# Kernel tuning notes

Measured on AMD Instinct MI355X. Metric: run time of the kernel, lower is better.

Reference implementation:

```python
import jax, jax.numpy as jnp
import numpy as np
import math

N_EMBD = 1024
N_HEAD = 16
HEAD_DIM = N_EMBD // N_HEAD


def setup_inputs() -> dict:
    key = jax.random.key(0)
    k_x, k_w1, k_b1, k_w2, k_b2 = jax.random.split(key, 5)
    B, T = 2, 2048
    x = jax.random.normal(k_x, (B, T, N_EMBD), dtype=jnp.float32)
    # ln1: Linear(n_embd, 3*n_embd); weights stored as [in, out] for x @ W
    W_qkv = jax.random.normal(k_w1, (N_EMBD, 3 * N_EMBD), dtype=jnp.float32) * 0.02
    b_qkv = jax.random.normal(k_b1, (3 * N_EMBD,), dtype=jnp.float32) * 0.02
    # ln2: Linear(n_embd, n_embd)
    W_out = jax.random.normal(k_w2, (N_EMBD, N_EMBD), dtype=jnp.float32) * 0.02
    b_out = jax.random.normal(k_b2, (N_EMBD,), dtype=jnp.float32) * 0.02
    return {"x": x, "W_qkv": W_qkv, "b_qkv": b_qkv, "W_out": W_out, "b_out": b_out}


def reference(x, W_qkv, b_qkv, W_out, b_out):
    B, T, C = x.shape
    qkv = x @ W_qkv + b_qkv                      # [B,T,3C]
    q, k, v = jnp.split(qkv, 3, axis=-1)
    # reshape to heads: [B, H, T, D]
    def to_heads(t):
        return t.reshape(B, T, N_HEAD, HEAD_DIM).transpose(0, 2, 1, 3)
    Q, K, V = to_heads(q), to_heads(k), to_heads(v)
    # NOTE: scale is 1/sqrt(n_head), as in the source (not sqrt(head_dim));
    # NOTE: no causal mask is applied, faithfully matching the source forward.
    scale = 1.0 / math.sqrt(N_HEAD)
    scores = jnp.einsum('bhqd,bhkd->bhqk', Q, K) * scale  # [B,H,T,T]
    attn = jax.nn.softmax(scores, axis=-1)
    out = jnp.einsum('bhqk,bhkd->bhqd', attn, V)          # [B,H,T,D]
    out = out.transpose(0, 2, 1, 3).reshape(B, T, C)
    # dropout = 0.0 -> identity (eval mode)
    return out @ W_out + b_out
```

## Files before the change

kernel.cpp:

```cpp
#include <hip/hip_runtime.h>
#include <hip/hip_bf16.h>
#include <stdint.h>

typedef __bf16 bf16_t;
typedef __bf16 bf16x8 __attribute__((ext_vector_type(8)));
typedef float  f32x4  __attribute__((ext_vector_type(4)));

#define AS1 __attribute__((address_space(1)))
#define AS3 __attribute__((address_space(3)))

__device__ __forceinline__ void gload16(const bf16_t* g, char* l) {
  __builtin_amdgcn_global_load_lds((AS1 const void*)(uintptr_t)g, (AS3 void*)l, 16, 0, 0);
}
__device__ __forceinline__ int swz8(int r) { return (r & 7) ^ ((r >> 2) & 6); }

#define C2S 0.36067376022224085f

__global__ __launch_bounds__(256) void prep(
    const float* __restrict__ x, const float* __restrict__ Wqkv, const float* __restrict__ Wout,
    bf16_t* __restrict__ xb, bf16_t* __restrict__ wqkvT, bf16_t* __restrict__ woutT) {
  __shared__ float tile[32][33];
  const int bid = blockIdx.x, tid = threadIdx.x;
  if (bid < 4096) {
    const int i = bid * 256 + tid;
    float4 v = reinterpret_cast<const float4*>(x)[i];
    union { bf16_t h[4]; unsigned long long u; } r;
    r.h[0] = (bf16_t)v.x; r.h[1] = (bf16_t)v.y; r.h[2] = (bf16_t)v.z; r.h[3] = (bf16_t)v.w;
    reinterpret_cast<unsigned long long*>(xb)[i] = r.u;
    return;
  }
  const float* W; bf16_t* Wt; int N, tb;
  if (bid < 7168) { W = Wqkv; Wt = wqkvT; N = 3072; tb = bid - 4096; }
  else            { W = Wout; Wt = woutT; N = 1024; tb = bid - 7168; }
  const int kb = (tb & 31) * 32, nb = (tb >> 5) * 32;
  const int tx = tid & 31, ty = tid >> 5;
#pragma unroll
  for (int i = 0; i < 32; i += 8)
    tile[ty + i][tx] = W[(size_t)(kb + ty + i) * N + nb + tx];
  __syncthreads();
#pragma unroll
  for (int i = 0; i < 32; i += 8)
    Wt[(size_t)(nb + ty + i) * 1024 + kb + tx] = (bf16_t)tile[tx][ty + i];
}

template<int MI>
__global__ __launch_bounds__(256) void gemm_bt(
    const bf16_t* __restrict__ A, const bf16_t* __restrict__ Bt,
    const float* __restrict__ bias,
    bf16_t* __restrict__ outb, bf16_t* __restrict__ vtb, float* __restrict__ outf,
    int M, int N, int K, int ldo, int mode) {
  __shared__ bf16_t lA[2][MI * 1024];
  __shared__ bf16_t lB[2][4096];
  const int tid = threadIdx.x;
  const int wave = tid >> 6, lane = tid & 63;
  const int lr = lane & 15, lg = lane >> 4;
  const int ntiles = N >> 7;
  const int bid = (blockIdx.x & 7) * ((int)gridDim.x >> 3) + (blockIdx.x >> 3);
  const int bn = bid % ntiles, bm = bid / ntiles;
  const int m0 = bm * (MI * 32), n0 = bn * 128;
  const int wr = wave >> 1, wc = wave & 1;
  f32x4 acc[MI][4] = {};

  auto stageg = [&](int buf, int k0) {
#pragma unroll
    for (int it = 0; it < MI / 2; ++it) {
      const int wbase = it * 256 + wave * 64;
      const int lam = wbase + lane;
      const int row = lam >> 2;
      const int colb = ((lam & 3) << 4) ^ (((row >> 1) & 3) << 4);
      gload16(A + (size_t)(m0 + row) * K + k0 + (colb >> 1), (char*)&lA[buf][0] + wbase * 16);
    }
#pragma unroll
    for (int it = 0; it < 2; ++it) {
      const int wbase = it * 256 + wave * 64;
      const int lam = wbase + lane;
      const int row = lam >> 2;
      const int colb = ((lam & 3) << 4) ^ (((row >> 1) & 3) << 4);
      gload16(Bt + (size_t)(n0 + row) * K + k0 + (colb >> 1), (char*)&lB[buf][0] + wbase * 16);
    }
  };

  stageg(0, 0);
  __syncthreads();
  int cur = 0;

  for (int k0 = 0; k0 < K; k0 += 32) {
    if (k0 + 32 < K) stageg(cur ^ 1, k0 + 32);

    const char* pA = (const char*)&lA[cur][0];
    const char* pB = (const char*)&lB[cur][0];
    bf16x8 af[MI], bfv[4];
#pragma unroll
    for (int mi = 0; mi < MI; ++mi) {
      const int row = wr * (MI * 16) + mi * 16 + lr;
      af[mi] = *reinterpret_cast<const bf16x8*>(
          pA + row * 64 + ((lg * 16) ^ (((row >> 1) & 3) << 4)));
    }
#pragma unroll
    for (int ni = 0; ni < 4; ++ni) {
      const int row = wc * 64 + ni * 16 + lr;
      bfv[ni] = *reinterpret_cast<const bf16x8*>(
          pB + row * 64 + ((lg * 16) ^ (((row >> 1) & 3) << 4)));
    }
    __builtin_amdgcn_s_setprio(1);
#pragma unroll
    for (int mi = 0; mi < MI; ++mi)
#pragma unroll
      for (int ni = 0; ni < 4; ++ni)
        acc[mi][ni] = __builtin_amdgcn_mfma_f32_16x16x32_bf16(af[mi], bfv[ni], acc[mi][ni], 0, 0, 0);
    __builtin_amdgcn_s_setprio(0);

    __syncthreads();
    cur ^= 1;
  }

#pragma unroll
  for (int mi = 0; mi < MI; ++mi) {
#pragma unroll
    for (int ni = 0; ni < 4; ++ni) {
      const int col = n0 + wc * 64 + ni * 16 + lr;
      const float bv = bias[col];
      const int rg0 = m0 + wr * (MI * 16) + mi * 16 + lg * 4;
      if (mode == 1 && col >= 2048) {
        const int colv = col - 2048;
        const int dd = colv & 63, hh = colv >> 6;
        const int bb = rg0 >> 11, t = rg0 & 2047;
        union { bf16_t h4[4]; unsigned long long u; } pk;
#pragma unroll
        for (int r = 0; r < 4; ++r) pk.h4[r] = (bf16_t)(acc[mi][ni][r] + bv);
        *reinterpret_cast<unsigned long long*>(
            vtb + (size_t)(bb * 16 + hh) * 131072 + (size_t)dd * 2048 + t) = pk.u;
      } else {
        const float sc = (mode == 1 && col < 1024) ? C2S : 1.f;
#pragma unroll
        for (int r = 0; r < 4; ++r) {
          const float v = (acc[mi][ni][r] + bv) * sc;
          if (mode == 2) outf[(size_t)(rg0 + r) * ldo + col] = v;
          else           outb[(size_t)(rg0 + r) * ldo + col] = (bf16_t)v;
        }
      }
    }
  }
}

__global__ __launch_bounds__(512) void attn_fwd(
    const bf16_t* __restrict__ qkv2,
    const bf16_t* __restrict__ vT,
    bf16_t* __restrict__ a0, bf16_t* __restrict__ a1,
    float* __restrict__ lbuf) {
  __shared__ bf16_t lds[2][8192];
  const int tid = threadIdx.x;
  const int wave = tid >> 6, lane = tid & 63;
  const int lr = lane & 15, lg = lane >> 4;
  const int id = blockIdx.x;
  const int xcd = id & 7, slot = id >> 3;
  const int bh = xcd * 4 + (slot & 3);
  const int rest = slot >> 2;
  const int qb = rest & 7, kvh = rest >> 3;
  const int b = bh >> 4, h = bh & 15;

  const int q0 = qb * 256 + wave * 32;
  const bf16_t* Qp = qkv2 + (size_t)(b * 2048 + q0) * 2048 + h * 64;
  bf16x8 qf[2][2];
#pragma unroll
  for (int hx = 0; hx < 2; ++hx) {
    qf[hx][0] = *reinterpret_cast<const bf16x8*>(Qp + (size_t)(hx * 16 + lr) * 2048 + lg * 8);
    qf[hx][1] = *reinterpret_cast<const bf16x8*>(Qp + (size_t)(hx * 16 + lr) * 2048 + 32 + lg * 8);
  }

  const int kr = tid >> 3;
  const int ks = (tid & 7) ^ swz8(kr);
  const bf16_t* Ksrc = qkv2 + (size_t)(b * 2048 + kvh * 1024 + kr) * 2048 + 1024 + h * 64 + ks * 8;
  const bf16_t* Vsrc = vT + (size_t)bh * 131072 + (size_t)kr * 2048 + kvh * 1024 + ks * 8;

  auto stage = [&](int buf, int kb) {
    char* base = (char*)&lds[buf][0] + wave * 1024;
    gload16(Ksrc + (size_t)kb * 131072, base);
    gload16(Vsrc + (size_t)kb * 64, base + 8192);
  };

  int kofs[4][2], vofs[4][2];
#pragma unroll
  for (int t = 0; t < 4; ++t) {
    const int kk = 32 * (t >> 1) + 8 * (lr >> 2) + 4 * (t & 1) + (lr & 3);
    const int sw = swz8(kk) << 4;
    kofs[t][0] = (kk << 7) + ((lg * 16) ^ sw);
    kofs[t][1] = (kk << 7) + ((64 + lg * 16) ^ sw);
  }
#pragma unroll
  for (int nc = 0; nc < 4; ++nc) {
    const int vr = nc * 16 + lr;
    const int sw = swz8(vr) << 4;
    vofs[nc][0] = 8192 + (vr << 7) + ((lg * 16) ^ sw);
    vofs[nc][1] = 8192 + (vr << 7) + ((64 + lg * 16) ^ sw);
  }

  f32x4 acc[2][4] = {};
  f32x4 accl[2] = {};
  bf16x8 ones;
#pragma unroll
  for (int j = 0; j < 8; ++j) ones[j] = (bf16_t)1.0f;

  int cur = 0;
  stage(0, 0);
  __syncthreads();

  for (int kb = 0; kb < 16; ++kb) {
    if (kb < 15) stage(cur ^ 1, kb + 1);
    const char* bK = (const char*)&lds[cur][0];

    f32x4 s[2][4];
#pragma unroll
    for (int t = 0; t < 4; ++t) {
      const bf16x8 k0 = *reinterpret_cast<const bf16x8*>(bK + kofs[t][0]);
      const bf16x8 k1 = *reinterpret_cast<const bf16x8*>(bK + kofs[t][1]);
#pragma unroll
      for (int hx = 0; hx < 2; ++hx) {
        f32x4 z = {0.f, 0.f, 0.f, 0.f};
        z = __builtin_amdgcn_mfma_f32_16x16x32_bf16(k0, qf[hx][0], z, 0, 0, 0);
        s[hx][t] = __builtin_amdgcn_mfma_f32_16x16x32_bf16(k1, qf[hx][1], z, 0, 0, 0);
      }
    }

    bf16x8 pa[2][2];
#pragma unroll
    for (int hx = 0; hx < 2; ++hx) {
      float p[16];
#pragma unroll
      for (int t = 0; t < 4; ++t)
#pragma unroll
        for (int r = 0; r < 4; ++r)
          p[t * 4 + r] = __builtin_amdgcn_exp2f(s[hx][t][r]);
#pragma unroll
      for (int j = 0; j < 8; ++j) { pa[hx][0][j] = (bf16_t)p[j]; pa[hx][1][j] = (bf16_t)p[8 + j]; }
    }

    __builtin_amdgcn_s_setprio(1);
#pragma unroll
    for (int hx = 0; hx < 2; ++hx) {
      accl[hx] = __builtin_amdgcn_mfma_f32_16x16x32_bf16(pa[hx][0], ones, accl[hx], 0, 0, 0);
      accl[hx] = __builtin_amdgcn_mfma_f32_16x16x32_bf16(pa[hx][1], ones, accl[hx], 0, 0, 0);
    }

#pragma unroll
    for (int nc = 0; nc < 4; ++nc) {
      const bf16x8 v0 = *reinterpret_cast<const bf16x8*>(bK + vofs[nc][0]);
      const bf16x8 v1 = *reinterpret_cast<const bf16x8*>(bK + vofs[nc][1]);
#pragma unroll
      for (int hx = 0; hx < 2; ++hx) {
        acc[hx][nc] = __builtin_amdgcn_mfma_f32_16x16x32_bf16(pa[hx][0], v0, acc[hx][nc], 0, 0, 0);
        acc[hx][nc] = __builtin_amdgcn_mfma_f32_16x16x32_bf16(pa[hx][1], v1, acc[hx][nc], 0, 0, 0);
      }
    }
    __builtin_amdgcn_s_setprio(0);

    __syncthreads();
    cur ^= 1;
  }

  bf16_t* ap = kvh ? a1 : a0;
#pragma unroll
  for (int hx = 0; hx < 2; ++hx) {
#pragma unroll
    for (int r = 0; r < 4; ++r) {
      const float lf = 1.f / accl[hx][r];
      const int qg = q0 + hx * 16 + lg * 4 + r;
      bf16_t* op = ap + (size_t)(b * 2048 + qg) * 1024 + h * 64 + lr;
#pragma unroll
      for (int nc = 0; nc < 4; ++nc) op[nc * 16] = (bf16_t)(acc[hx][nc][r] * lf);
      if (lr == 0)
        lbuf[(size_t)(kvh * 4096 + b * 2048 + qg) * 16 + h] = accl[hx][r];
    }
  }
}

__global__ void attn_reduce(const bf16_t* __restrict__ a0, const bf16_t* __restrict__ a1,
                            const float* __restrict__ lbuf, bf16_t* __restrict__ aout) {
  const int i = blockIdx.x * 256 + threadIdx.x;
  const int r = i >> 7, h = (i & 127) >> 3;
  const float l0 = lbuf[(size_t)r * 16 + h];
  const float l1 = lbuf[(size_t)(4096 + r) * 16 + h];
  const float inv = 1.f / (l0 + l1);
  const float w0 = l0 * inv, w1 = l1 * inv;
  const bf16x8 v0 = reinterpret_cast<const bf16x8*>(a0)[i];
  const bf16x8 v1 = reinterpret_cast<const bf16x8*>(a1)[i];
  bf16x8 o;
#pragma unroll
  for (int j = 0; j < 8; ++j) o[j] = (bf16_t)(w0 * (float)v0[j] + w1 * (float)v1[j]);
  reinterpret_cast<bf16x8*>(aout)[i] = o;
}

extern "C" void kernel_launch(void* const* d_in, const int* in_sizes, int n_in,
                              void* d_out, int out_size, void* d_ws, size_t ws_size,
                              hipStream_t stream) {
  (void)in_sizes; (void)n_in; (void)out_size; (void)ws_size;
  const float* x    = (const float*)d_in[0];
  const float* Wqkv = (const float*)d_in[1];
  const float* bqkv = (const float*)d_in[2];
  const float* Wout = (const float*)d_in[3];
  const float* bout = (const float*)d_in[4];
  float* out = (float*)d_out;

  char* ws = (char*)d_ws;
  bf16_t* xb    = (bf16_t*)(ws);
  bf16_t* a0    = (bf16_t*)(ws);
  bf16_t* wqkvT = (bf16_t*)(ws + 8388608);
  bf16_t* woutT = (bf16_t*)(ws + 14680064);
  bf16_t* qkv2  = (bf16_t*)(ws + 16777216);
  bf16_t* aout  = (bf16_t*)(ws + 16777216);
  bf16_t* vT    = (bf16_t*)(ws + 33554432);
  bf16_t* a1    = (bf16_t*)(ws + 41943040);
  float*  lbuf  = (float*)(ws + 50331648);

  prep<<<8192, 256, 0, stream>>>(x, Wqkv, Wout, xb, wqkvT, woutT);
  gemm_bt<4><<<768, 256, 0, stream>>>(xb, wqkvT, bqkv, qkv2, vT, nullptr, 4096, 3072, 1024, 2048, 1);
  attn_fwd<<<512, 512, 0, stream>>>(qkv2, vT, a0, a1, lbuf);
  attn_reduce<<<2048, 256, 0, stream>>>(a0, a1, lbuf, aout);
  gemm_bt<2><<<512, 256, 0, stream>>>(aout, woutT, bout, nullptr, nullptr, out, 4096, 1024, 1024, 1024, 2);
}
```

Before: 112.4 us.

## Triple-buffer LDS staging with partial vmcnt waits in GEMM and attention

Moves the GEMM and attention kernels from double to triple LDS buffering. Two tiles are prefetched ahead, and explicit s_waitcnt vmcnt counts plus raw s_barrier wait only for the tile in use, replacing the full __syncthreads drain. This hides more global-to-LDS latency behind MFMA work. In exchange it uses 1.5x the LDS per block, which can lower occupancy, and the hardcoded vmcnt values must match the exact number of loads issued per stage.

```diff
diff --git a/kernel.cpp b/kernel.cpp
--- a/kernel.cpp
+++ b/kernel.cpp
@@ -49,8 +49,8 @@
     const float* __restrict__ bias,
     bf16_t* __restrict__ outb, bf16_t* __restrict__ vtb, float* __restrict__ outf,
     int M, int N, int K, int ldo, int mode) {
-  __shared__ bf16_t lA[2][MI * 1024];
-  __shared__ bf16_t lB[2][4096];
+  __shared__ bf16_t lA[3][MI * 1024];
+  __shared__ bf16_t lB[3][4096];
   const int tid = threadIdx.x;
   const int wave = tid >> 6, lane = tid & 63;
   const int lr = lane & 15, lg = lane >> 4;
@@ -80,12 +80,24 @@
     }
   };
 
+  const int nt = K >> 5;
   stageg(0, 0);
-  __syncthreads();
-  int cur = 0;
-
-  for (int k0 = 0; k0 < K; k0 += 32) {
-    if (k0 + 32 < K) stageg(cur ^ 1, k0 + 32);
+  stageg(1, 32);
+  int cur = 0, stg = 2;
+
+  for (int t = 0; t < nt; ++t) {
+    if (t + 2 < nt) stageg(stg, (t + 2) << 5);
+    if (t + 2 < nt) {
+      if constexpr (MI == 4) asm volatile("s_waitcnt vmcnt(8)" ::: "memory");
+      else                   asm volatile("s_waitcnt vmcnt(6)" ::: "memory");
+    } else if (t + 1 < nt) {
+      if constexpr (MI == 4) asm volatile("s_waitcnt vmcnt(4)" ::: "memory");
+      else                   asm volatile("s_waitcnt vmcnt(3)" ::: "memory");
+    } else {
+      asm volatile("s_waitcnt vmcnt(0)" ::: "memory");
+    }
+    __builtin_amdgcn_s_barrier();
+    __builtin_amdgcn_sched_barrier(0);
 
     const char* pA = (const char*)&lA[cur][0];
     const char* pB = (const char*)&lB[cur][0];
@@ -110,8 +122,10 @@
         acc[mi][ni] = __builtin_amdgcn_mfma_f32_16x16x32_bf16(af[mi], bfv[ni], acc[mi][ni], 0, 0, 0);
     __builtin_amdgcn_s_setprio(0);
 
-    __syncthreads();
-    cur ^= 1;
+    __builtin_amdgcn_sched_barrier(0);
+    __builtin_amdgcn_s_barrier();
+    cur = cur == 2 ? 0 : cur + 1;
+    stg = stg == 2 ? 0 : stg + 1;
   }
 
 #pragma unroll
@@ -148,7 +162,7 @@
     const bf16_t* __restrict__ vT,
     bf16_t* __restrict__ a0, bf16_t* __restrict__ a1,
     float* __restrict__ lbuf) {
-  __shared__ bf16_t lds[2][8192];
+  __shared__ bf16_t lds[3][8192];
   const int tid = threadIdx.x;
   const int wave = tid >> 6, lane = tid & 63;
   const int lr = lane & 15, lg = lane >> 4;
@@ -201,12 +215,17 @@
 #pragma unroll
   for (int j = 0; j < 8; ++j) ones[j] = (bf16_t)1.0f;
 
-  int cur = 0;
   stage(0, 0);
-  __syncthreads();
+  stage(1, 1);
+  int cur = 0, stg = 2;
 
   for (int kb = 0; kb < 16; ++kb) {
-    if (kb < 15) stage(cur ^ 1, kb + 1);
+    if (kb + 2 < 16) stage(stg, kb + 2);
+    if (kb + 2 < 16)      asm volatile("s_waitcnt vmcnt(4)" ::: "memory");
+    else if (kb + 1 < 16) asm volatile("s_waitcnt vmcnt(2)" ::: "memory");
+    else                  asm volatile("s_waitcnt vmcnt(0)" ::: "memory");
+    __builtin_amdgcn_s_barrier();
+    __builtin_amdgcn_sched_barrier(0);
     const char* bK = (const char*)&lds[cur][0];
 
     f32x4 s[2][4];
@@ -254,8 +273,10 @@
     }
     __builtin_amdgcn_s_setprio(0);
 
-    __syncthreads();
-    cur ^= 1;
+    __builtin_amdgcn_sched_barrier(0);
+    __builtin_amdgcn_s_barrier();
+    cur = cur == 2 ? 0 : cur + 1;
+    stg = stg == 2 ? 0 : stg + 1;
   }
 
   bf16_t* ap = kvh ? a1 : a0;
```

Result: no change. 113.9 us (+1.3%).
